# Kernel optimization log

Measured on AMD Instinct MI355X. Metric: run time of the kernel, lower is better.

## Reference

```python
import jax, jax.numpy as jnp
import numpy as np

H = 51  # hidden size hard-coded in the module

def lstm_cell(x, h, c, W_ih, W_hh, b_ih, b_hh):
    # PyTorch LSTMCell: gates = x @ W_ih^T + b_ih + h @ W_hh^T + b_hh
    g = x @ W_ih.T + h @ W_hh.T + (b_ih + b_hh)  # [B, 4H]
    i, f, gg, o = jnp.split(g, 4, axis=-1)
    c_new = jax.nn.sigmoid(f) * c + jax.nn.sigmoid(i) * jnp.tanh(gg)
    h_new = jax.nn.sigmoid(o) * jnp.tanh(c_new)
    return h_new, c_new

def setup_inputs() -> dict:
    key = jax.random.key(0)
    ks = jax.random.split(key, 12)
    B, T = 2048, 2048
    s1 = 1.0 / np.sqrt(H)
    u = lambda k, shape: jax.random.uniform(k, shape, jnp.float32, -s1, s1)
    return {
        "input": jax.random.normal(ks[0], (B, T), jnp.float32),
        "W_ih1": u(ks[1], (4 * H, 1)),
        "W_hh1": u(ks[2], (4 * H, H)),
        "b_ih1": u(ks[3], (4 * H,)),
        "b_hh1": u(ks[4], (4 * H,)),
        "W_ih2": u(ks[5], (4 * H, H)),
        "W_hh2": u(ks[6], (4 * H, H)),
        "b_ih2": u(ks[7], (4 * H,)),
        "b_hh2": u(ks[8], (4 * H,)),
        "W_lin": u(ks[9], (1, H)),
        "b_lin": u(ks[10], (1,)),
    }

def reference(input, W_ih1, W_hh1, b_ih1, b_hh1, W_ih2, W_hh2, b_ih2, b_hh2, W_lin, b_lin):
    B, T = input.shape
    xs = input.T[:, :, None]  # [T, B, 1]
    h1 = jnp.zeros((B, H), input.dtype)
    c1 = jnp.zeros((B, H), input.dtype)
    h2 = jnp.zeros((B, H), input.dtype)
    c2 = jnp.zeros((B, H), input.dtype)

    def step(carry, x_t):
        h1, c1, h2, c2 = carry
        h1, c1 = lstm_cell(x_t, h1, c1, W_ih1, W_hh1, b_ih1, b_hh1)
        h2, c2 = lstm_cell(h1, h2, c2, W_ih2, W_hh2, b_ih2, b_hh2)
        y = h2 @ W_lin.T + b_lin  # [B, 1]
        return (h1, c1, h2, c2), y[:, 0]

    _, ys = jax.lax.scan(step, (h1, c1, h2, c2), xs)  # ys: [T, B]
    return ys.T  # [B, T]
```

## Files before the change

### kernel.cpp

```cpp
#include <hip/hip_runtime.h>

#define H 51
#define TSEQ 2048
#define BB 16
#define THREADS 1024

typedef _Float16 __attribute__((ext_vector_type(8))) half8;
typedef float    __attribute__((ext_vector_type(4))) float4v;

#define LOG2E    1.44269504f
#define TWOLOG2E 2.88539008f

__device__ __forceinline__ float lstm_ew(float4v a, float& c) {
    float eA = __builtin_amdgcn_exp2f(-a[0]);
    float eB = __builtin_amdgcn_exp2f(a[2]);
    float eF = __builtin_amdgcn_exp2f(-a[1]);
    float pA = eA + 1.0f, pB = eB + 1.0f, pF = eF + 1.0f;
    float dAB = pA * pB;
    float num = fmaf(c, dAB, (eB - 1.0f) * pF);
    float r   = __builtin_amdgcn_rcpf(dAB * pF);
    float cn  = num * r;
    c = cn;
    float uD = fminf(cn * TWOLOG2E, 126.0f);
    float eD = __builtin_amdgcn_exp2f(uD);
    float eC = __builtin_amdgcn_exp2f(-a[3]);
    float r2 = __builtin_amdgcn_rcpf((eC + 1.0f) * (eD + 1.0f));
    return (eD - 1.0f) * r2;
}

__global__ __launch_bounds__(THREADS)
void lstm_w16b_kernel(const float* __restrict__ input,
                      const float* __restrict__ W_ih1, const float* __restrict__ W_hh1,
                      const float* __restrict__ b_ih1, const float* __restrict__ b_hh1,
                      const float* __restrict__ W_ih2, const float* __restrict__ W_hh2,
                      const float* __restrict__ b_ih2, const float* __restrict__ b_hh2,
                      const float* __restrict__ W_lin, const float* __restrict__ b_lin,
                      float* __restrict__ out)
{
    __shared__ half8 hb1[2][2][64];
    __shared__ half8 hb2[2][2][64];
    __shared__ float h2f[2][64 * 16];
    __shared__ float xss[2][64 * 17];
    __shared__ float ybf[BB][64];
    __shared__ float wlin[H + 1];

    const int tid  = threadIdx.x;
    const int wv   = tid >> 6;
    const int lane = tid & 63;
    const int n    = lane & 15;
    const int qd   = lane >> 4;
    const int b0   = blockIdx.x * BB;

    if (tid < 256) {
        half8 z = {0,0,0,0,0,0,0,0};
        (&hb1[0][0][0])[tid] = z;
        (&hb2[0][0][0])[tid] = z;
    }
    if (tid < H)  wlin[tid] = W_lin[tid];
    if (tid == H) wlin[H]   = b_lin[0];

    if (wv == 15) {
#pragma unroll
        for (int k = 0; k < 16; ++k)
            xss[0][lane * 17 + k] = input[(size_t)(b0 + k) * TSEQ + lane];
    }

    half8 wa1[2];
    half8 wa2[4];
    {
        const int tw1 = (wv < 12) ? wv : ((wv == 13) ? 12 : 13);
        const int tw2 = (wv < 12) ? wv : ((wv == 14) ? 12 : 13);
        {
            const int arow = tw1 * 16 + n;
            const int cell = arow >> 2, gate = arow & 3;
            const int orow = gate * H + cell;
            const float gsc = (gate == 2) ? TWOLOG2E : LOG2E;
            const bool rok = (arow < 4 * H);
#pragma unroll
            for (int s = 0; s < 2; ++s)
#pragma unroll
                for (int j = 0; j < 8; ++j) {
                    int kk = s * 32 + qd * 8 + j;
                    wa1[s][j] = (_Float16)((rok && kk < H) ? gsc * W_hh1[orow * H + kk] : 0.f);
                }
        }
        {
            const int arow = tw2 * 16 + n;
            const int cell = arow >> 2, gate = arow & 3;
            const int orow = gate * H + cell;
            const float gsc = (gate == 2) ? TWOLOG2E : LOG2E;
            const bool rok = (arow < 4 * H);
#pragma unroll
            for (int s = 0; s < 4; ++s)
#pragma unroll
                for (int j = 0; j < 8; ++j) {
                    int kk = s * 32 + qd * 8 + j;
                    float w = 0.f;
                    if (rok) {
                        if (kk < H)                       w = gsc * W_ih2[orow * H + kk];
                        else if (kk >= 64 && kk < 64 + H) w = gsc * W_hh2[orow * H + (kk - 64)];
                    }
                    wa2[s][j] = (_Float16)w;
                }
        }
    }

    const int ewv = (wv == 13 || wv == 14) ? 12 : ((wv < 12) ? wv : 13);
    const int jj  = ewv * 4 + qd;
    float4v bias1v, wih1v, bias2v;
    {
        const bool cok1 = (jj < H) && (wv < 12 || wv == 13);
        const bool cok2 = (jj < H) && (wv < 12 || wv == 14);
#pragma unroll
        for (int r = 0; r < 4; ++r) {
            const float gsc = (r == 2) ? TWOLOG2E : LOG2E;
            const int orow = r * H + jj;
            bias1v[r] = cok1 ? gsc * (b_ih1[orow] + b_hh1[orow]) : 0.f;
            wih1v[r]  = cok1 ? gsc * W_ih1[orow] : 0.f;
            bias2v[r] = cok2 ? gsc * (b_ih2[orow] + b_hh2[orow]) : 0.f;
        }
    }

    float c1 = 0.f, c2 = 0.f;
    const int js = jj >> 5, jq = (jj & 31) >> 3, j7 = jj & 7;

    __syncthreads();

    if (wv < 12 || wv == 13) {
        const float xb = xss[0][n];
        float4v a;
#pragma unroll
        for (int r = 0; r < 4; ++r) a[r] = fmaf(wih1v[r], xb, bias1v[r]);
        float h = lstm_ew(a, c1);
        ((_Float16*)&hb1[0][js][jq * 16 + n])[j7] = (_Float16)h;
    }
    __syncthreads();

#define STEP(t, P)                                                              \
    {                                                                           \
        if (wv < 12) {                                                          \
            half8 g1[2], g2[2];                                                 \
            g1[0] = hb1[P][0][lane];      g1[1] = hb1[P][1][lane];              \
            g2[0] = hb2[P ^ 1][0][lane];  g2[1] = hb2[P ^ 1][1][lane];          \
                      \
            const int t1 = (t) + 1;                                             \
            const float xb = xss[(t1 >> 6) & 1][(t1 & 63) * 17 + n];            \
            float4v a1;                                                         \
            _Pragma("unroll")                                                   \
            for (int r = 0; r < 4; ++r) a1[r] = fmaf(wih1v[r], xb, bias1v[r]);  \
            a1 = __builtin_amdgcn_mfma_f32_16x16x32_f16(wa1[0], g1[0], a1, 0, 0, 0); \
            a1 = __builtin_amdgcn_mfma_f32_16x16x32_f16(wa1[1], g1[1], a1, 0, 0, 0); \
            float4v a2a = bias2v;                                               \
            float4v a2b = (float4v){0.f, 0.f, 0.f, 0.f};                        \
            a2a = __builtin_amdgcn_mfma_f32_16x16x32_f16(wa2[0], g1[0], a2a, 0, 0, 0); \
            a2b = __builtin_amdgcn_mfma_f32_16x16x32_f16(wa2[2], g2[0], a2b, 0, 0, 0); \
            a2a = __builtin_amdgcn_mfma_f32_16x16x32_f16(wa2[1], g1[1], a2a, 0, 0, 0); \
            a2b = __builtin_amdgcn_mfma_f32_16x16x32_f16(wa2[3], g2[1], a2b, 0, 0, 0); \
                                          \
            {                                                                   \
                float h = lstm_ew(a1, c1);                                      \
                ((_Float16*)&hb1[P ^ 1][js][jq * 16 + n])[j7] = (_Float16)h;    \
            }                                                                   \
                                                     \
            {                                                                   \
                float4v a2;                                                     \
                _Pragma("unroll")                                               \
                for (int r = 0; r < 4; ++r) a2[r] = a2a[r] + a2b[r];            \
                float h = lstm_ew(a2, c2);                                      \
                ((_Float16*)&hb2[P][js][jq * 16 + n])[j7] = (_Float16)h;        \
                h2f[P][jj * 16 + n] = h;                                        \
            }                                                                   \
        } else if (wv == 12) {                                                  \
                                                                    \
            if ((t) > 0) {                                                      \
                const int b = lane & 15, kg = lane >> 4;                        \
                float a = 0.f;                                                  \
                _Pragma("unroll")                                               \
                for (int it = 0; it < 13; ++it) {                               \
                    int j = kg + it * 4;                                        \
                    if (j < H) a = fmaf(wlin[j], h2f[P ^ 1][j * 16 + b], a);    \
                }                                                               \
                a += __shfl_xor(a, 16, 64);                                     \
                a += __shfl_xor(a, 32, 64);                                     \
                if (kg == 0) ybf[b][((t) - 1) & 63] = a + wlin[H];              \
                if (((t) & 63) == 0) {                                          \
                    int tb = (t) - 64;                                          \
                    _Pragma("unroll")                                           \
                    for (int r = 0; r < BB; ++r)                                \
                        out[(size_t)(b0 + r) * TSEQ + tb + lane] = ybf[r][lane]; \
                }                                                               \
            }                                                                   \
        } else if (wv == 13) {                                                  \
                 \
            half8 g1[2];                                                        \
            g1[0] = hb1[P][0][lane];      g1[1] = hb1[P][1][lane];              \
            const int t1 = (t) + 1;                                             \
            const float xb = xss[(t1 >> 6) & 1][(t1 & 63) * 17 + n];            \
            float4v a1;                                                         \
            _Pragma("unroll")                                                   \
            for (int r = 0; r < 4; ++r) a1[r] = fmaf(wih1v[r], xb, bias1v[r]);  \
            a1 = __builtin_amdgcn_mfma_f32_16x16x32_f16(wa1[0], g1[0], a1, 0, 0, 0); \
            a1 = __builtin_amdgcn_mfma_f32_16x16x32_f16(wa1[1], g1[1], a1, 0, 0, 0); \
            float h = lstm_ew(a1, c1);                                          \
            ((_Float16*)&hb1[P ^ 1][js][jq * 16 + n])[j7] = (_Float16)h;        \
        } else if (wv == 14) {                                                  \
                                                     \
            half8 g1[2], g2[2];                                                 \
            g1[0] = hb1[P][0][lane];      g1[1] = hb1[P][1][lane];              \
            g2[0] = hb2[P ^ 1][0][lane];  g2[1] = hb2[P ^ 1][1][lane];          \
            float4v a2a = bias2v;                                               \
            float4v a2b = (float4v){0.f, 0.f, 0.f, 0.f};                        \
            a2a = __builtin_amdgcn_mfma_f32_16x16x32_f16(wa2[0], g1[0], a2a, 0, 0, 0); \
            a2b = __builtin_amdgcn_mfma_f32_16x16x32_f16(wa2[2], g2[0], a2b, 0, 0, 0); \
            a2a = __builtin_amdgcn_mfma_f32_16x16x32_f16(wa2[1], g1[1], a2a, 0, 0, 0); \
            a2b = __builtin_amdgcn_mfma_f32_16x16x32_f16(wa2[3], g2[1], a2b, 0, 0, 0); \
            float4v a2;                                                         \
            _Pragma("unroll")                                                   \
            for (int r = 0; r < 4; ++r) a2[r] = a2a[r] + a2b[r];                \
            float h = lstm_ew(a2, c2);                                          \
            ((_Float16*)&hb2[P][js][jq * 16 + n])[j7] = (_Float16)h;            \
            h2f[P][jj * 16 + n] = h;                                            \
        } else {                                                                \
                                       \
            if (((t) & 63) == 32 && (t) + 32 < TSEQ) {                          \
                const int cp = ((t) >> 6) & 1;                                  \
                _Pragma("unroll")                                               \
                for (int k = 0; k < 16; ++k)                                    \
                    xss[cp ^ 1][lane * 17 + k] =                                \
                        input[(size_t)(b0 + k) * TSEQ + ((t) + 32) + lane];     \
            }                                                                   \
        }                                                                       \
        __syncthreads();                                                        \
    }

#pragma unroll 1
    for (int t = 0; t < TSEQ; t += 2) {
        STEP(t, 0)
        STEP(t + 1, 1)
    }
#undef STEP

    if (wv == 12) {
        const int b = lane & 15, kg = lane >> 4;
        float a = 0.f;
#pragma unroll
        for (int it = 0; it < 13; ++it) {
            int j = kg + it * 4;
            if (j < H) a = fmaf(wlin[j], h2f[1][j * 16 + b], a);
        }
        a += __shfl_xor(a, 16, 64);
        a += __shfl_xor(a, 32, 64);
        if (kg == 0) ybf[b][63] = a + wlin[H];
#pragma unroll
        for (int r = 0; r < BB; ++r)
            out[(size_t)(b0 + r) * TSEQ + (TSEQ - 64) + lane] = ybf[r][lane];
    }
}

extern "C" void kernel_launch(void* const* d_in, const int* in_sizes, int n_in,
                              void* d_out, int out_size, void* d_ws, size_t ws_size,
                              hipStream_t stream) {
    const float* input = (const float*)d_in[0];
    const float* W_ih1 = (const float*)d_in[1];
    const float* W_hh1 = (const float*)d_in[2];
    const float* b_ih1 = (const float*)d_in[3];
    const float* b_hh1 = (const float*)d_in[4];
    const float* W_ih2 = (const float*)d_in[5];
    const float* W_hh2 = (const float*)d_in[6];
    const float* b_ih2 = (const float*)d_in[7];
    const float* b_hh2 = (const float*)d_in[8];
    const float* W_lin = (const float*)d_in[9];
    const float* b_lin = (const float*)d_in[10];

    lstm_w16b_kernel<<<dim3(2048 / BB), dim3(THREADS), 0, stream>>>(
        input, W_ih1, W_hh1, b_ih1, b_hh1,
        W_ih2, W_hh2, b_ih2, b_hh2, W_lin, b_lin,
        (float*)d_out);
}
```

Before: 1.410 ms.

## Fold output linear into layer-2 MFMA padding row and raise MFMA wave priority

Puts the W_lin weights into the unused padding row (arow 204) of the layer-2 weight tile, so the output projection comes out of the MFMA that wave 14 already runs. This removes the h2f staging buffer, the per-step scalar dot product in wave 12 and the wlin shared array. The y ring buffer now holds 128 steps and is flushed every 64 steps. s_setprio is also raised around the compute sections of the recurrent waves so they win issue slots over the store and prefetch waves. The trade-off is that the output is computed from the fp16 h2 in the previous-step buffer, which lowers its precision, and the ring indexing is more involved.

```diff
diff --git a/kernel.cpp b/kernel.cpp
--- a/kernel.cpp
+++ b/kernel.cpp
@@ -39,10 +39,8 @@
 {
     __shared__ half8 hb1[2][2][64];
     __shared__ half8 hb2[2][2][64];
-    __shared__ float h2f[2][64 * 16];
     __shared__ float xss[2][64 * 17];
-    __shared__ float ybf[BB][64];
-    __shared__ float wlin[H + 1];
+    __shared__ float ybf[128][17];
 
     const int tid  = threadIdx.x;
     const int wv   = tid >> 6;
@@ -50,14 +48,13 @@
     const int n    = lane & 15;
     const int qd   = lane >> 4;
     const int b0   = blockIdx.x * BB;
+    const float blin = b_lin[0];
 
     if (tid < 256) {
         half8 z = {0,0,0,0,0,0,0,0};
         (&hb1[0][0][0])[tid] = z;
         (&hb2[0][0][0])[tid] = z;
     }
-    if (tid < H)  wlin[tid] = W_lin[tid];
-    if (tid == H) wlin[H]   = b_lin[0];
 
     if (wv == 15) {
 #pragma unroll
@@ -99,6 +96,8 @@
                     if (rok) {
                         if (kk < H)                       w = gsc * W_ih2[orow * H + kk];
                         else if (kk >= 64 && kk < 64 + H) w = gsc * W_hh2[orow * H + (kk - 64)];
+                    } else if (arow == 204) {
+                        if (kk >= 64 && kk < 64 + H)      w = W_lin[kk - 64];
                     }
                     wa2[s][j] = (_Float16)w;
                 }
@@ -139,6 +138,7 @@
 #define STEP(t, P)                                                              \
     {                                                                           \
         if (wv < 12) {                                                          \
+            __builtin_amdgcn_s_setprio(1);                                      \
             half8 g1[2], g2[2];                                                 \
             g1[0] = hb1[P][0][lane];      g1[1] = hb1[P][1][lane];              \
             g2[0] = hb2[P ^ 1][0][lane];  g2[1] = hb2[P ^ 1][1][lane];          \
@@ -161,37 +161,28 @@
                 float h = lstm_ew(a1, c1);                                      \
                 ((_Float16*)&hb1[P ^ 1][js][jq * 16 + n])[j7] = (_Float16)h;    \
             }                                                                   \
-                                                     \
+                                                             \
             {                                                                   \
                 float4v a2;                                                     \
                 _Pragma("unroll")                                               \
                 for (int r = 0; r < 4; ++r) a2[r] = a2a[r] + a2b[r];            \
                 float h = lstm_ew(a2, c2);                                      \
                 ((_Float16*)&hb2[P][js][jq * 16 + n])[j7] = (_Float16)h;        \
-                h2f[P][jj * 16 + n] = h;                                        \
-            }                                                                   \
+            }                                                                   \
+            __builtin_amdgcn_s_setprio(0);                                      \
         } else if (wv == 12) {                                                  \
-                                                                    \
-            if ((t) > 0) {                                                      \
-                const int b = lane & 15, kg = lane >> 4;                        \
-                float a = 0.f;                                                  \
+             \
+             \
+            if ((t) > 64 && ((t) & 63) == 1) {                                  \
+                const int tb = (t) - 65;                                        \
+                const int sb = tb & 127;                                        \
                 _Pragma("unroll")                                               \
-                for (int it = 0; it < 13; ++it) {                               \
-                    int j = kg + it * 4;                                        \
-                    if (j < H) a = fmaf(wlin[j], h2f[P ^ 1][j * 16 + b], a);    \
-                }                                                               \
-                a += __shfl_xor(a, 16, 64);                                     \
-                a += __shfl_xor(a, 32, 64);                                     \
-                if (kg == 0) ybf[b][((t) - 1) & 63] = a + wlin[H];              \
-                if (((t) & 63) == 0) {                                          \
-                    int tb = (t) - 64;                                          \
-                    _Pragma("unroll")                                           \
-                    for (int r = 0; r < BB; ++r)                                \
-                        out[(size_t)(b0 + r) * TSEQ + tb + lane] = ybf[r][lane]; \
-                }                                                               \
+                for (int r = 0; r < BB; ++r)                                    \
+                    out[(size_t)(b0 + r) * TSEQ + tb + lane] = ybf[sb + lane][r]; \
             }                                                                   \
         } else if (wv == 13) {                                                  \
                  \
+            __builtin_amdgcn_s_setprio(1);                                      \
             half8 g1[2];                                                        \
             g1[0] = hb1[P][0][lane];      g1[1] = hb1[P][1][lane];              \
             const int t1 = (t) + 1;                                             \
@@ -203,8 +194,10 @@
             a1 = __builtin_amdgcn_mfma_f32_16x16x32_f16(wa1[1], g1[1], a1, 0, 0, 0); \
             float h = lstm_ew(a1, c1);                                          \
             ((_Float16*)&hb1[P ^ 1][js][jq * 16 + n])[j7] = (_Float16)h;        \
+            __builtin_amdgcn_s_setprio(0);                                      \
         } else if (wv == 14) {                                                  \
-                                                     \
+                       \
+            __builtin_amdgcn_s_setprio(1);                                      \
             half8 g1[2], g2[2];                                                 \
             g1[0] = hb1[P][0][lane];      g1[1] = hb1[P][1][lane];              \
             g2[0] = hb2[P ^ 1][0][lane];  g2[1] = hb2[P ^ 1][1][lane];          \
@@ -219,7 +212,8 @@
             for (int r = 0; r < 4; ++r) a2[r] = a2a[r] + a2b[r];                \
             float h = lstm_ew(a2, c2);                                          \
             ((_Float16*)&hb2[P][js][jq * 16 + n])[j7] = (_Float16)h;            \
-            h2f[P][jj * 16 + n] = h;                                            \
+            if (qd == 3) ybf[((t) - 1) & 127][n] = a2[0] + blin;    \
+            __builtin_amdgcn_s_setprio(0);                                      \
         } else {                                                                \
                                        \
             if (((t) & 63) == 32 && (t) + 32 < TSEQ) {                          \
@@ -240,20 +234,19 @@
     }
 #undef STEP
 
+    if (wv == 14) {
+        half8 g2a = hb2[1][0][lane], g2b = hb2[1][1][lane];
+        float4v yb = (float4v){0.f, 0.f, 0.f, 0.f};
+        yb = __builtin_amdgcn_mfma_f32_16x16x32_f16(wa2[2], g2a, yb, 0, 0, 0);
+        yb = __builtin_amdgcn_mfma_f32_16x16x32_f16(wa2[3], g2b, yb, 0, 0, 0);
+        if (qd == 3) ybf[127][n] = yb[0] + blin;
+    }
+    __syncthreads();
     if (wv == 12) {
-        const int b = lane & 15, kg = lane >> 4;
-        float a = 0.f;
-#pragma unroll
-        for (int it = 0; it < 13; ++it) {
-            int j = kg + it * 4;
-            if (j < H) a = fmaf(wlin[j], h2f[1][j * 16 + b], a);
-        }
-        a += __shfl_xor(a, 16, 64);
-        a += __shfl_xor(a, 32, 64);
-        if (kg == 0) ybf[b][63] = a + wlin[H];
+        const int tb = TSEQ - 64;
 #pragma unroll
         for (int r = 0; r < BB; ++r)
-            out[(size_t)(b0 + r) * TSEQ + (TSEQ - 64) + lane] = ybf[r][lane];
+            out[(size_t)(b0 + r) * TSEQ + tb + lane] = ybf[64 + lane][r];
     }
 }
 
```

Result: no change. 1.420 ms (+0.7%).
